# Optimization experiments

Measured on AMD Instinct MI355X. Metric: run time of the kernel, lower is better.

The kernel has to match this reference:

```python
import jax, jax.numpy as jnp
import numpy as np

N = 10000
E = 160000
DIMS = [512, 512, 512, 256]  # in -> hidden -> hidden -> out (num_layers=3)
EPS = 1e-12  # F.normalize default eps


def _sage_layer(x, edge_index, Wl, b, Wr):
    # PyG SAGEConv (mean aggr, normalize=True):
    # out = lin_l(mean_{j in N(i)} x_j) + lin_r(x_i), then L2-normalize rows.
    src = edge_index[0]
    dst = edge_index[1]
    msg = x[src]  # [E, d] gather of source-node features
    agg = jax.ops.segment_sum(msg, dst, num_segments=N)  # [N, d]
    cnt = jax.ops.segment_sum(jnp.ones((E,), x.dtype), dst, num_segments=N)
    mean = agg / jnp.maximum(cnt, 1.0)[:, None]
    out = mean @ Wl.T + b + x @ Wr.T
    norm = jnp.sqrt(jnp.sum(out * out, axis=-1, keepdims=True))
    return out / jnp.maximum(norm, EPS)


def setup_inputs() -> dict:
    key = jax.random.key(0)
    ks = jax.random.split(key, 2 + 3 * len(DIMS))
    x = jax.random.normal(ks[0], (N, DIMS[0]), dtype=jnp.float32)
    edge_index = jax.random.randint(ks[1], (2, E), 0, N, dtype=jnp.int64)
    inp = {"x": x, "edge_index": edge_index}
    k = 2
    for i in range(len(DIMS) - 1):
        din, dout = DIMS[i], DIMS[i + 1]
        s = 1.0 / np.sqrt(din)
        inp[f"Wl{i}"] = jax.random.uniform(ks[k], (dout, din), jnp.float32, -s, s); k += 1
        inp[f"b{i}"] = jax.random.uniform(ks[k], (dout,), jnp.float32, -s, s); k += 1
        inp[f"Wr{i}"] = jax.random.uniform(ks[k], (dout, din), jnp.float32, -s, s); k += 1
    return inp


def reference(x, edge_index, Wl0, b0, Wr0, Wl1, b1, Wr1, Wl2, b2, Wr2):
    params = [(Wl0, b0, Wr0), (Wl1, b1, Wr1), (Wl2, b2, Wr2)]
    for Wl, b, Wr in params:
        x = _sage_layer(x, edge_index, Wl, b, Wr)
        x = jax.nn.relu(x)
        # F.dropout(training=False) is identity at inference
    return x
```

## Files before the change

### kernel.cpp

```cpp
#include <hip/hip_runtime.h>

#define NN 10000

typedef __attribute__((ext_vector_type(8))) short short8;
typedef __attribute__((ext_vector_type(4))) float f32x4;

__device__ __forceinline__ ushort f2b(float f) {
    union { float f; uint32_t u; } v; v.f = f;
    uint32_t u = v.u;
    return (ushort)((u + 0x7fffu + ((u >> 16) & 1u)) >> 16);
}
__device__ __forceinline__ uint packbf(float a, float b) {
    return (uint)f2b(a) | ((uint)f2b(b) << 16);
}
__device__ __forceinline__ float blo(uint u) {
    union { uint u; float f; } v; v.u = u << 16; return v.f;
}
__device__ __forceinline__ float bhi(uint u) {
    union { uint u; float f; } v; v.u = u & 0xffff0000u; return v.f;
}

__global__ __launch_bounds__(256) void zero_int(int* __restrict__ p, int n) {
    int i = blockIdx.x * 256 + threadIdx.x;
    if (i < n) p[i] = 0;
}

__global__ __launch_bounds__(256) void count_dst(const int* __restrict__ dst,
                                                 int* __restrict__ counts, int E) {
    int i = blockIdx.x * 256 + threadIdx.x;
    if (i < E) atomicAdd(&counts[dst[i]], 1);
}

__global__ __launch_bounds__(1024) void scan_build(const int* __restrict__ counts,
                                                   int* __restrict__ offsets,
                                                   int* __restrict__ cursor,
                                                   float* __restrict__ inv_cnt, int n) {
    __shared__ int part[1024];
    int tid = threadIdx.x;
    int per = (n + 1023) / 1024;
    int base = tid * per;
    int s = 0;
    for (int i = 0; i < per; i++) { int idx = base + i; if (idx < n) s += counts[idx]; }
    part[tid] = s;
    __syncthreads();
    for (int off = 1; off < 1024; off <<= 1) {
        int v = (tid >= off) ? part[tid - off] : 0;
        __syncthreads();
        part[tid] += v;
        __syncthreads();
    }
    int run = (tid > 0) ? part[tid - 1] : 0;
    for (int i = 0; i < per; i++) {
        int idx = base + i;
        if (idx < n) {
            int c = counts[idx];
            offsets[idx] = run;
            cursor[idx]  = run;
            inv_cnt[idx] = 1.0f / fmaxf((float)c, 1.0f);
            run += c;
        }
    }
}

__global__ __launch_bounds__(256) void scatter_edges(const int* __restrict__ src,
                                                     const int* __restrict__ dst,
                                                     int* __restrict__ cursor,
                                                     int* __restrict__ sorted_src, int E) {
    int i = blockIdx.x * 256 + threadIdx.x;
    if (i < E) {
        int p = atomicAdd(&cursor[dst[i]], 1);
        sorted_src[p] = src[i];
    }
}

__global__ __launch_bounds__(256) void cvt_all(const float* __restrict__ x,
                                               const float* __restrict__ Wl0,
                                               const float* __restrict__ Wr0,
                                               const float* __restrict__ Wl1,
                                               const float* __restrict__ Wr1,
                                               const float* __restrict__ Wl2,
                                               const float* __restrict__ Wr2,
                                               ushort* __restrict__ xbuf,
                                               ushort* __restrict__ Wc0,
                                               ushort* __restrict__ Wc1,
                                               ushort* __restrict__ Wc2) {
    int i = blockIdx.x * 256 + threadIdx.x;
    const float* src;
    ushort* dst;
    if (i < 1280000) {
        int idx = i * 4;
        src = x + idx;
        dst = xbuf + idx;
    } else if (i < 1411072) {
        int j = (i - 1280000) * 4;
        int row = j >> 9, col = j & 511;
        src = (row < 512) ? (Wl0 + (size_t)row * 512 + col)
                          : (Wr0 + (size_t)(row - 512) * 512 + col);
        dst = Wc0 + j;
    } else if (i < 1542144) {
        int j = (i - 1411072) * 4;
        int row = j >> 9, col = j & 511;
        src = (row < 512) ? (Wl1 + (size_t)row * 512 + col)
                          : (Wr1 + (size_t)(row - 512) * 512 + col);
        dst = Wc1 + j;
    } else if (i < 1607680) {
        int j = (i - 1542144) * 4;
        int row = j >> 9, col = j & 511;
        src = (row < 256) ? (Wl2 + (size_t)row * 512 + col)
                          : (Wr2 + (size_t)(row - 256) * 512 + col);
        dst = Wc2 + j;
    } else {
        return;
    }
    float4 v = *(const float4*)src;
    uint2 p;
    p.x = packbf(v.x, v.y);
    p.y = packbf(v.z, v.w);
    *(uint2*)dst = p;
}

__global__ __launch_bounds__(256) void gemm_split(const ushort* __restrict__ A,
                                                  const ushort* __restrict__ B,
                                                  ushort* __restrict__ G,
                                                  float* __restrict__ R,
                                                  int M, int dout) {
    __shared__ ushort Asl[2][128 * 32];
    __shared__ ushort Bsl[2][128 * 32];
    const int tid  = threadIdx.x;
    const int w    = tid >> 6;
    const int lane = tid & 63;

    const int nbx = gridDim.x, nby = gridDim.y;
    const int nwg = nbx * nby;
    const int id  = blockIdx.y * nbx + blockIdx.x;
    const int qq  = nwg >> 3, rr = nwg & 7;
    const int xcd = id & 7, blk = id >> 3;
    const int swzid = (xcd < rr ? xcd * (qq + 1) : rr * (qq + 1) + (xcd - rr) * qq) + blk;
    const int bx = swzid % nbx, by = swzid / nbx;

    const int bm = by * 128, bn = bx * 128;
    const int wm = (w & 1) * 64, wn = (w >> 1) * 64;
    const int row16 = lane & 15, q = lane >> 4;

    f32x4 acc[4][4];
#pragma unroll
    for (int i = 0; i < 4; i++)
#pragma unroll
        for (int j = 0; j < 4; j++) acc[i][j] = (f32x4){0.f, 0.f, 0.f, 0.f};

    const int sc_r = lane >> 2;
    const int sc_s = lane & 3;
    const int koff = sc_s ^ ((sc_r >> 1) & 3);
    const int swz  = (row16 >> 1) & 3;

    auto stage = [&](int buf, int k0) {
#pragma unroll
        for (int c = 0; c < 2; c++) {
            int chunk = w * 2 + c;
            int rloc  = chunk * 16 + sc_r;
            int growA = bm + rloc; growA = growA < M ? growA : M - 1;
            const ushort* gpA = A + (size_t)growA * 512 + k0 + koff * 8;
            __builtin_amdgcn_global_load_lds(
                (const __attribute__((address_space(1))) uint32_t*)gpA,
                (__attribute__((address_space(3))) uint32_t*)&Asl[buf][chunk * 512],
                16, 0, 0);
            const ushort* gpB = B + (size_t)(bn + rloc) * 512 + k0 + koff * 8;
            __builtin_amdgcn_global_load_lds(
                (const __attribute__((address_space(1))) uint32_t*)gpB,
                (__attribute__((address_space(3))) uint32_t*)&Bsl[buf][chunk * 512],
                16, 0, 0);
        }
    };

    const int NT = 512 / 32;
    stage(0, 0);
    __syncthreads();
    int cur = 0;

    for (int t = 0; t < NT; ++t) {
        if (t + 1 < NT) stage(cur ^ 1, (t + 1) * 32);

        short8 af[4], bfr[4];
        int s = q ^ swz;
#pragma unroll
        for (int i = 0; i < 4; i++) {
            int r = wm + i * 16 + row16;
            af[i] = *(const short8*)&Asl[cur][r * 32 + s * 8];
        }
#pragma unroll
        for (int j = 0; j < 4; j++) {
            int rn = wn + j * 16 + row16;
            bfr[j] = *(const short8*)&Bsl[cur][rn * 32 + s * 8];
        }
#pragma unroll
        for (int i = 0; i < 4; i++)
#pragma unroll
            for (int j = 0; j < 4; j++)
                acc[i][j] = __builtin_amdgcn_mfma_f32_16x16x32_bf16(
                    af[i], bfr[j], acc[i][j], 0, 0, 0);

        __syncthreads();
        cur ^= 1;
    }

    const bool isR = (bn >= dout);
#pragma unroll
    for (int i = 0; i < 4; i++) {
#pragma unroll
        for (int r2 = 0; r2 < 4; r2++) {
            int row = bm + wm + i * 16 + q * 4 + r2;
            if (row < M) {
                if (isR) {
                    float* Rp = R + (size_t)row * dout + (bn - dout) + wn + row16;
#pragma unroll
                    for (int j = 0; j < 4; j++)
                        Rp[j * 16] = acc[i][j][r2];
                } else {
                    ushort* Gp = G + (size_t)row * dout + bn + wn + row16;
#pragma unroll
                    for (int j = 0; j < 4; j++)
                        Gp[j * 16] = f2b(acc[i][j][r2]);
                }
            }
        }
    }
}

template <int DOUT, bool FINAL>
__global__ __launch_bounds__(256) void aggfin(const ushort* __restrict__ G,
                                              const float* __restrict__ R,
                                              const float* __restrict__ bias,
                                              const int* __restrict__ offsets,
                                              const int* __restrict__ counts,
                                              const int* __restrict__ sorted_src,
                                              const float* __restrict__ inv_cnt,
                                              ushort* __restrict__ xnext,
                                              float* __restrict__ outf, int n) {
    constexpr int PL = DOUT / 64;
    int wave = threadIdx.x >> 6;
    int lane = threadIdx.x & 63;
    int node = blockIdx.x * 4 + wave;
    if (node >= n) return;
    int start = offsets[node];
    int cnt   = counts[node];
    float inv = inv_cnt[node];

    float acc[PL];
#pragma unroll
    for (int k = 0; k < PL; k++) acc[k] = 0.f;

    if constexpr (DOUT == 512) {
        const uint* gp = (const uint*)G + lane * 4;
#define ACC8(v) do { \
        acc[0] += blo(v.x); acc[1] += bhi(v.x); \
        acc[2] += blo(v.y); acc[3] += bhi(v.y); \
        acc[4] += blo(v.z); acc[5] += bhi(v.z); \
        acc[6] += blo(v.w); acc[7] += bhi(v.w); } while (0)
        int e = 0;
        for (; e + 8 <= cnt; e += 8) {
            uint4 vv[8];
#pragma unroll
            for (int u = 0; u < 8; u++) {
                int s0 = sorted_src[start + e + u];
                vv[u] = *(const uint4*)(gp + (size_t)s0 * 256);
            }
#pragma unroll
            for (int u = 0; u < 8; u++) ACC8(vv[u]);
        }
        for (; e < cnt; e++) {
            int s0 = sorted_src[start + e];
            uint4 v0 = *(const uint4*)(gp + (size_t)s0 * 256);
            ACC8(v0);
        }
#undef ACC8
    } else {
        const uint* gp = (const uint*)G + lane * 2;
#define ACC4(v) do { \
        acc[0] += blo(v.x); acc[1] += bhi(v.x); \
        acc[2] += blo(v.y); acc[3] += bhi(v.y); } while (0)
        int e = 0;
        for (; e + 8 <= cnt; e += 8) {
            uint2 vv[8];
#pragma unroll
            for (int u = 0; u < 8; u++) {
                int s0 = sorted_src[start + e + u];
                vv[u] = *(const uint2*)(gp + (size_t)s0 * 128);
            }
#pragma unroll
            for (int u = 0; u < 8; u++) ACC4(vv[u]);
        }
        for (; e < cnt; e++) {
            int s0 = sorted_src[start + e];
            uint2 v0 = *(const uint2*)(gp + (size_t)s0 * 128);
            ACC4(v0);
        }
#undef ACC4
    }

    float v[PL];
    const float* Rp = R + (size_t)node * DOUT + lane * PL;
    const float* Bp = bias + lane * PL;
#pragma unroll
    for (int k = 0; k < PL; k += 4) {
        float4 r4 = *(const float4*)(Rp + k);
        float4 b4 = *(const float4*)(Bp + k);
        v[k + 0] = acc[k + 0] * inv + r4.x + b4.x;
        v[k + 1] = acc[k + 1] * inv + r4.y + b4.y;
        v[k + 2] = acc[k + 2] * inv + r4.z + b4.z;
        v[k + 3] = acc[k + 3] * inv + r4.w + b4.w;
    }
    float ss = 0.f;
#pragma unroll
    for (int k = 0; k < PL; k++) ss += v[k] * v[k];
#pragma unroll
    for (int m = 32; m >= 1; m >>= 1) ss += __shfl_xor(ss, m, 64);
    float scale = 1.0f / fmaxf(sqrtf(ss), 1e-12f);

    if constexpr (FINAL) {
        float* Op = outf + (size_t)node * DOUT + lane * PL;
#pragma unroll
        for (int k = 0; k < PL; k += 4) {
            float4 o;
            o.x = fmaxf(v[k + 0] * scale, 0.f);
            o.y = fmaxf(v[k + 1] * scale, 0.f);
            o.z = fmaxf(v[k + 2] * scale, 0.f);
            o.w = fmaxf(v[k + 3] * scale, 0.f);
            *(float4*)(Op + k) = o;
        }
    } else {
        uint4 o;
        float r0 = fmaxf(v[0] * scale, 0.f), r1 = fmaxf(v[1] * scale, 0.f);
        float r2 = fmaxf(v[2] * scale, 0.f), r3 = fmaxf(v[3] * scale, 0.f);
        float r4 = fmaxf(v[4] * scale, 0.f), r5 = fmaxf(v[5] * scale, 0.f);
        float r6 = fmaxf(v[6] * scale, 0.f), r7 = fmaxf(v[7] * scale, 0.f);
        o.x = packbf(r0, r1); o.y = packbf(r2, r3);
        o.z = packbf(r4, r5); o.w = packbf(r6, r7);
        *(uint4*)(xnext + (size_t)node * 512 + lane * 8) = o;
    }
}

extern "C" void kernel_launch(void* const* d_in, const int* in_sizes, int n_in,
                              void* d_out, int out_size, void* d_ws, size_t ws_size,
                              hipStream_t stream) {
    const float* x    = (const float*)d_in[0];
    const int*   edge = (const int*)d_in[1];
    const float* Wl0  = (const float*)d_in[2];
    const float* b0   = (const float*)d_in[3];
    const float* Wr0  = (const float*)d_in[4];
    const float* Wl1  = (const float*)d_in[5];
    const float* b1   = (const float*)d_in[6];
    const float* Wr1  = (const float*)d_in[7];
    const float* Wl2  = (const float*)d_in[8];
    const float* b2   = (const float*)d_in[9];
    const float* Wr2  = (const float*)d_in[10];

    const int E = in_sizes[1] / 2;

    char* ws = (char*)d_ws;
    int*    counts  = (int*)(ws + 0);
    int*    offsets = (int*)(ws + 40960);
    int*    cursor  = (int*)(ws + 81920);
    float*  invc    = (float*)(ws + 122880);
    int*    sorted  = (int*)(ws + 163840);
    ushort* Wc0     = (ushort*)(ws + 819200);
    ushort* Wc1     = (ushort*)(ws + 1867776);
    ushort* Wc2     = (ushort*)(ws + 2916352);
    ushort* xbuf    = (ushort*)(ws + 3440640);
    ushort* Gbuf    = (ushort*)(ws + 13680640);
    float*  Rbuf    = (float*)(ws + 23920640);

    zero_int<<<(NN + 255) / 256, 256, 0, stream>>>(counts, NN);
    count_dst<<<(E + 255) / 256, 256, 0, stream>>>(edge + E, counts, E);
    scan_build<<<1, 1024, 0, stream>>>(counts, offsets, cursor, invc, NN);
    scatter_edges<<<(E + 255) / 256, 256, 0, stream>>>(edge, edge + E, cursor, sorted, E);

    cvt_all<<<(1607680 + 255) / 256, 256, 0, stream>>>(x, Wl0, Wr0, Wl1, Wr1, Wl2, Wr2,
                                                       xbuf, Wc0, Wc1, Wc2);

    const int gyM = (NN + 127) / 128;
    const int gb  = (NN + 3) / 4;

    gemm_split<<<dim3(8, gyM), 256, 0, stream>>>(xbuf, Wc0, Gbuf, Rbuf, NN, 512);
    aggfin<512, false><<<gb, 256, 0, stream>>>(Gbuf, Rbuf, b0, offsets, counts,
                                               sorted, invc, xbuf, nullptr, NN);
    gemm_split<<<dim3(8, gyM), 256, 0, stream>>>(xbuf, Wc1, Gbuf, Rbuf, NN, 512);
    aggfin<512, false><<<gb, 256, 0, stream>>>(Gbuf, Rbuf, b1, offsets, counts,
                                               sorted, invc, xbuf, nullptr, NN);
    gemm_split<<<dim3(4, gyM), 256, 0, stream>>>(xbuf, Wc2, Gbuf, Rbuf, NN, 256);
    aggfin<256, true><<<gb, 256, 0, stream>>>(Gbuf, Rbuf, b2, offsets, counts,
                                              sorted, invc, nullptr, (float*)d_out, NN);
}
```

Baseline: 251.6 us.

## Pad neighbor lists to multiples of eight and double-buffer aggregation gathers

The CSR neighbor lists are padded to multiples of eight, with the padding pointing at a zeroed dummy row (index NN) in the G buffers. This removes the scalar tail loop. The aggregation loop now double-buffers its batches of eight gathers, issuing the next batch's loads before accumulating the current one to hide memory latency. The R and bias loads are hoisted before the gather loop, and a separate G2 buffer is added for the 256-wide layer so its padding row stays correct. In exchange, register pressure rises and some wasted loads of the zero row are added.

```diff
diff --git a/kernel.cpp b/kernel.cpp
--- a/kernel.cpp
+++ b/kernel.cpp
@@ -34,13 +34,17 @@
 __global__ __launch_bounds__(1024) void scan_build(const int* __restrict__ counts,
                                                    int* __restrict__ offsets,
                                                    int* __restrict__ cursor,
-                                                   float* __restrict__ inv_cnt, int n) {
+                                                   float* __restrict__ inv_cnt,
+                                                   int* __restrict__ sorted_src, int n) {
     __shared__ int part[1024];
     int tid = threadIdx.x;
     int per = (n + 1023) / 1024;
     int base = tid * per;
     int s = 0;
-    for (int i = 0; i < per; i++) { int idx = base + i; if (idx < n) s += counts[idx]; }
+    for (int i = 0; i < per; i++) {
+        int idx = base + i;
+        if (idx < n) s += (counts[idx] + 7) & ~7;
+    }
     part[tid] = s;
     __syncthreads();
     for (int off = 1; off < 1024; off <<= 1) {
@@ -53,11 +57,13 @@
     for (int i = 0; i < per; i++) {
         int idx = base + i;
         if (idx < n) {
-            int c = counts[idx];
+            int c    = counts[idx];
+            int cpad = (c + 7) & ~7;
             offsets[idx] = run;
             cursor[idx]  = run;
             inv_cnt[idx] = 1.0f / fmaxf((float)c, 1.0f);
-            run += c;
+            for (int j = c; j < cpad; j++) sorted_src[run + j] = NN;
+            run += cpad;
         }
     }
 }
@@ -83,7 +89,9 @@
                                                ushort* __restrict__ xbuf,
                                                ushort* __restrict__ Wc0,
                                                ushort* __restrict__ Wc1,
-                                               ushort* __restrict__ Wc2) {
+                                               ushort* __restrict__ Wc2,
+                                               ushort* __restrict__ Gbuf,
+                                               ushort* __restrict__ G2) {
     int i = blockIdx.x * 256 + threadIdx.x;
     const float* src;
     ushort* dst;
@@ -109,6 +117,16 @@
         src = (row < 256) ? (Wl2 + (size_t)row * 512 + col)
                           : (Wr2 + (size_t)(row - 256) * 512 + col);
         dst = Wc2 + j;
+    } else if (i < 1607744) {
+        int t = i - 1607680;
+        uint4 z = {0, 0, 0, 0};
+        *(uint4*)(Gbuf + (size_t)NN * 512 + t * 8) = z;
+        return;
+    } else if (i < 1607776) {
+        int t = i - 1607744;
+        uint4 z = {0, 0, 0, 0};
+        *(uint4*)(G2 + (size_t)NN * 256 + t * 8) = z;
+        return;
     } else {
         return;
     }
@@ -244,6 +262,20 @@
     int start = offsets[node];
     int cnt   = counts[node];
     float inv = inv_cnt[node];
+    int nb    = ((cnt + 7) & ~7) >> 3;
+
+    float rv[PL], bv[PL];
+    {
+        const float* Rp = R + (size_t)node * DOUT + lane * PL;
+        const float* Bp = bias + lane * PL;
+#pragma unroll
+        for (int k = 0; k < PL; k += 4) {
+            float4 r4 = *(const float4*)(Rp + k);
+            float4 b4 = *(const float4*)(Bp + k);
+            rv[k + 0] = r4.x; rv[k + 1] = r4.y; rv[k + 2] = r4.z; rv[k + 3] = r4.w;
+            bv[k + 0] = b4.x; bv[k + 1] = b4.y; bv[k + 2] = b4.z; bv[k + 3] = b4.w;
+        }
+    }
 
     float acc[PL];
 #pragma unroll
@@ -251,64 +283,78 @@
 
     if constexpr (DOUT == 512) {
         const uint* gp = (const uint*)G + lane * 4;
+        uint4 va[8], vb[8];
+        auto load8 = [&](uint4* v, int e0) {
+#pragma unroll
+            for (int u = 0; u < 8; u++) {
+                int s0 = sorted_src[start + e0 + u];
+                v[u] = *(const uint4*)(gp + (size_t)s0 * 256);
+            }
+        };
 #define ACC8(v) do { \
         acc[0] += blo(v.x); acc[1] += bhi(v.x); \
         acc[2] += blo(v.y); acc[3] += bhi(v.y); \
         acc[4] += blo(v.z); acc[5] += bhi(v.z); \
         acc[6] += blo(v.w); acc[7] += bhi(v.w); } while (0)
-        int e = 0;
-        for (; e + 8 <= cnt; e += 8) {
-            uint4 vv[8];
-#pragma unroll
-            for (int u = 0; u < 8; u++) {
-                int s0 = sorted_src[start + e + u];
-                vv[u] = *(const uint4*)(gp + (size_t)s0 * 256);
-            }
-#pragma unroll
-            for (int u = 0; u < 8; u++) ACC8(vv[u]);
-        }
-        for (; e < cnt; e++) {
-            int s0 = sorted_src[start + e];
-            uint4 v0 = *(const uint4*)(gp + (size_t)s0 * 256);
-            ACC8(v0);
-        }
+        auto acc8v = [&](const uint4* v) {
+#pragma unroll
+            for (int u = 0; u < 8; u++) ACC8(v[u]);
+        };
 #undef ACC8
+        if (nb > 0) load8(va, 0);
+        int b = 1;
+        for (; b + 1 < nb; b += 2) {
+            load8(vb, b * 8);
+            acc8v(va);
+            load8(va, (b + 1) * 8);
+            acc8v(vb);
+        }
+        if (b < nb) {
+            load8(vb, b * 8);
+            acc8v(va);
+            acc8v(vb);
+        } else if (nb > 0) {
+            acc8v(va);
+        }
     } else {
         const uint* gp = (const uint*)G + lane * 2;
+        uint2 va[8], vb[8];
+        auto load8 = [&](uint2* v, int e0) {
+#pragma unroll
+            for (int u = 0; u < 8; u++) {
+                int s0 = sorted_src[start + e0 + u];
+                v[u] = *(const uint2*)(gp + (size_t)s0 * 128);
+            }
+        };
 #define ACC4(v) do { \
         acc[0] += blo(v.x); acc[1] += bhi(v.x); \
         acc[2] += blo(v.y); acc[3] += bhi(v.y); } while (0)
-        int e = 0;
-        for (; e + 8 <= cnt; e += 8) {
-            uint2 vv[8];
-#pragma unroll
-            for (int u = 0; u < 8; u++) {
-                int s0 = sorted_src[start + e + u];
-                vv[u] = *(const uint2*)(gp + (size_t)s0 * 128);
-            }
-#pragma unroll
-            for (int u = 0; u < 8; u++) ACC4(vv[u]);
-        }
-        for (; e < cnt; e++) {
-            int s0 = sorted_src[start + e];
-            uint2 v0 = *(const uint2*)(gp + (size_t)s0 * 128);
-            ACC4(v0);
-        }
+        auto acc8v = [&](const uint2* v) {
+#pragma unroll
+            for (int u = 0; u < 8; u++) ACC4(v[u]);
+        };
 #undef ACC4
+        if (nb > 0) load8(va, 0);
+        int b = 1;
+        for (; b + 1 < nb; b += 2) {
+            load8(vb, b * 8);
+            acc8v(va);
+            load8(va, (b + 1) * 8);
+            acc8v(vb);
+        }
+        if (b < nb) {
+            load8(vb, b * 8);
+            acc8v(va);
+            acc8v(vb);
+        } else if (nb > 0) {
+            acc8v(va);
+        }
     }
 
     float v[PL];
-    const float* Rp = R + (size_t)node * DOUT + lane * PL;
-    const float* Bp = bias + lane * PL;
-#pragma unroll
-    for (int k = 0; k < PL; k += 4) {
-        float4 r4 = *(const float4*)(Rp + k);
-        float4 b4 = *(const float4*)(Bp + k);
-        v[k + 0] = acc[k + 0] * inv + r4.x + b4.x;
-        v[k + 1] = acc[k + 1] * inv + r4.y + b4.y;
-        v[k + 2] = acc[k + 2] * inv + r4.z + b4.z;
-        v[k + 3] = acc[k + 3] * inv + r4.w + b4.w;
-    }
+#pragma unroll
+    for (int k = 0; k < PL; k++) v[k] = acc[k] * inv + rv[k] + bv[k];
+
     float ss = 0.f;
 #pragma unroll
     for (int k = 0; k < PL; k++) ss += v[k] * v[k];
@@ -362,20 +408,21 @@
     int*    cursor  = (int*)(ws + 81920);
     float*  invc    = (float*)(ws + 122880);
     int*    sorted  = (int*)(ws + 163840);
-    ushort* Wc0     = (ushort*)(ws + 819200);
-    ushort* Wc1     = (ushort*)(ws + 1867776);
-    ushort* Wc2     = (ushort*)(ws + 2916352);
-    ushort* xbuf    = (ushort*)(ws + 3440640);
-    ushort* Gbuf    = (ushort*)(ws + 13680640);
-    float*  Rbuf    = (float*)(ws + 23920640);
+    ushort* Wc0     = (ushort*)(ws + 1085440);
+    ushort* Wc1     = (ushort*)(ws + 2134016);
+    ushort* Wc2     = (ushort*)(ws + 3182592);
+    ushort* xbuf    = (ushort*)(ws + 3706880);
+    ushort* Gbuf    = (ushort*)(ws + 13946880);
+    ushort* G2      = (ushort*)(ws + 24188928);
+    float*  Rbuf    = (float*)(ws + 29309952);
 
     zero_int<<<(NN + 255) / 256, 256, 0, stream>>>(counts, NN);
     count_dst<<<(E + 255) / 256, 256, 0, stream>>>(edge + E, counts, E);
-    scan_build<<<1, 1024, 0, stream>>>(counts, offsets, cursor, invc, NN);
+    scan_build<<<1, 1024, 0, stream>>>(counts, offsets, cursor, invc, sorted, NN);
     scatter_edges<<<(E + 255) / 256, 256, 0, stream>>>(edge, edge + E, cursor, sorted, E);
 
-    cvt_all<<<(1607680 + 255) / 256, 256, 0, stream>>>(x, Wl0, Wr0, Wl1, Wr1, Wl2, Wr2,
-                                                       xbuf, Wc0, Wc1, Wc2);
+    cvt_all<<<(1607776 + 255) / 256, 256, 0, stream>>>(x, Wl0, Wr0, Wl1, Wr1, Wl2, Wr2,
+                                                       xbuf, Wc0, Wc1, Wc2, Gbuf, G2);
 
     const int gyM = (NN + 127) / 128;
     const int gb  = (NN + 3) / 4;
@@ -386,7 +433,7 @@
     gemm_split<<<dim3(8, gyM), 256, 0, stream>>>(xbuf, Wc1, Gbuf, Rbuf, NN, 512);
     aggfin<512, false><<<gb, 256, 0, stream>>>(Gbuf, Rbuf, b1, offsets, counts,
                                                sorted, invc, xbuf, nullptr, NN);
-    gemm_split<<<dim3(4, gyM), 256, 0, stream>>>(xbuf, Wc2, Gbuf, Rbuf, NN, 256);
-    aggfin<256, true><<<gb, 256, 0, stream>>>(Gbuf, Rbuf, b2, offsets, counts,
+    gemm_split<<<dim3(4, gyM), 256, 0, stream>>>(xbuf, Wc2, G2, Rbuf, NN, 256);
+    aggfin<256, true><<<gb, 256, 0, stream>>>(G2, Rbuf, b2, offsets, counts,
                                               sorted, invc, nullptr, (float*)d_out, NN);
 }
```

Result: no change. 256.4 us (+1.9%).
